# Kernel tuning notes

Measured on AMD Instinct MI355X. Metric: run time of the kernel, lower is better.

## Reference

```python
import jax, jax.numpy as jnp
import numpy as np

N = 50000
E = 800000
G_DIM = 512
H1 = 128
H2 = 128
R = 8  # 2 * n_speakers**2


def setup_inputs() -> dict:
    key = jax.random.key(0)
    ks = jax.random.split(key, 16)
    s = lambda d: 1.0 / np.sqrt(d)
    inp = {
        'node_features': jax.random.normal(ks[0], (N, G_DIM), jnp.float32),
        'edge_index': jax.random.randint(ks[1], (2, E), 0, N, jnp.int64),
        'edge_type': jax.random.randint(ks[2], (E,), 0, R, jnp.int64),
        # RGCNConv params
        'W_rel': jax.random.normal(ks[3], (R, G_DIM, H1), jnp.float32) * s(G_DIM),
        'W_root': jax.random.normal(ks[4], (G_DIM, H1), jnp.float32) * s(G_DIM),
        'b1': jnp.zeros((H1,), jnp.float32),
        # TransformerConv params (heads=1)
        'Wq': jax.random.normal(ks[5], (H1, H2), jnp.float32) * s(H1),
        'bq': jnp.zeros((H2,), jnp.float32),
        'Wk': jax.random.normal(ks[6], (H1, H2), jnp.float32) * s(H1),
        'bk': jnp.zeros((H2,), jnp.float32),
        'Wv': jax.random.normal(ks[7], (H1, H2), jnp.float32) * s(H1),
        'bv': jnp.zeros((H2,), jnp.float32),
        'Wskip': jax.random.normal(ks[8], (H1, H2), jnp.float32) * s(H1),
        'bskip': jnp.zeros((H2,), jnp.float32),
        # BatchNorm1d params
        'gamma': jnp.ones((H2,), jnp.float32),
        'beta': jnp.zeros((H2,), jnp.float32),
    }
    return inp


def reference(node_features, edge_index, edge_type, W_rel, W_root, b1,
              Wq, bq, Wk, bk, Wv, bv, Wskip, bskip, gamma, beta):
    n = node_features.shape[0]
    r = W_rel.shape[0]
    src, dst = edge_index[0], edge_index[1]

    # ---- RGCNConv: per-relation mean aggregation + root + bias ----
    # x @ W_r for all relations, then per-edge gather: [n,r,h1] -> [E,h1]
    xW = jnp.einsum('nf,rfh->nrh', node_features, W_rel)
    msg = xW[src, edge_type]                         # [E, H1]
    comp = dst * r + edge_type                       # composite (node, relation) key
    cnt = jax.ops.segment_sum(jnp.ones((msg.shape[0],), msg.dtype), comp,
                              num_segments=n * r)
    denom = jnp.maximum(cnt[comp], 1.0)[:, None]     # mean within each (node, rel)
    agg1 = jax.ops.segment_sum(msg / denom, dst, num_segments=n)
    h = agg1 + node_features @ W_root + b1           # [n, H1]

    # ---- TransformerConv (heads=1): segment-softmax attention ----
    q = h @ Wq + bq
    k = h @ Wk + bk
    v = h @ Wv + bv
    d = q.shape[-1]
    score = jnp.sum(q[dst] * k[src], axis=-1) / jnp.sqrt(jnp.float32(d))  # [E]
    smax = jax.ops.segment_max(score, dst, num_segments=n)
    smax = jnp.where(jnp.isfinite(smax), smax, 0.0)
    ex = jnp.exp(score - smax[dst])
    ssum = jax.ops.segment_sum(ex, dst, num_segments=n)
    alpha = ex / jnp.maximum(ssum[dst], 1e-16)       # [E]
    agg2 = jax.ops.segment_sum(alpha[:, None] * v[src], dst, num_segments=n)
    h2 = agg2 + h @ Wskip + bskip                    # root (lin_skip) path

    # ---- BatchNorm1d (training mode: batch stats) + LeakyReLU(0.01) ----
    mu = jnp.mean(h2, axis=0)
    var = jnp.mean((h2 - mu) ** 2, axis=0)
    xn = (h2 - mu) / jnp.sqrt(var + 1e-5)
    out = gamma * xn + beta
    return jnp.where(out >= 0, out, 0.01 * out)
```

## Files before the change

kernel.cpp:

```cpp
#include <hip/hip_runtime.h>

typedef float f32x4 __attribute__((ext_vector_type(4)));
typedef _Float16 f16x8 __attribute__((ext_vector_type(8)));

#define NN 50000
#define EE 800000
#define GD 512
#define H1C 128
#define RR 8
#define NC1 1152
#define NC2 512
#define SCAN_BLK 256
#define NCAST (NN * GD / 4)

__device__ __forceinline__ unsigned short f2h(float f){
  _Float16 h = (_Float16)f;
  unsigned short u; __builtin_memcpy(&u, &h, 2); return u;
}
__device__ __forceinline__ float h2f(unsigned short u){
  _Float16 h; __builtin_memcpy(&h, &u, 2); return (float)h;
}
__device__ __forceinline__ void gload16(const void* g, void* l){
  __builtin_amdgcn_global_load_lds(
      (const __attribute__((address_space(1))) unsigned int*)g,
      (__attribute__((address_space(3))) unsigned int*)l, 16, 0, 0);
}

__global__ void k_prep(unsigned* __restrict__ zp, int nzero,
                       const float* __restrict__ x, unsigned short* __restrict__ x16,
                       const float* __restrict__ W_rel, const float* __restrict__ W_root,
                       unsigned short* __restrict__ wcatT,
                       const float* __restrict__ Wq, const float* __restrict__ Wk,
                       const float* __restrict__ Wv, const float* __restrict__ Ws,
                       const float* __restrict__ bq, const float* __restrict__ bk,
                       const float* __restrict__ bv, const float* __restrict__ bs,
                       unsigned short* __restrict__ w2T, float* __restrict__ bias2){
  int i = blockIdx.x * 256 + threadIdx.x;
  if (i < nzero){ zp[i] = 0u; return; }
  i -= nzero;
  if (i < NCAST){
    int b = i * 4;
    float4 v = *(const float4*)(x + b);
    ushort4 o;
    o.x = f2h(v.x); o.y = f2h(v.y); o.z = f2h(v.z); o.w = f2h(v.w);
    *(ushort4*)(x16 + b) = o;
    return;
  }
  i -= NCAST;
  if (i < NC1 * GD){
    int j = i >> 9;
    int f = i & 511;
    float v;
    if (j < 1024) v = W_rel[((size_t)(j >> 7) * GD + f) * H1C + (j & 127)];
    else          v = W_root[(size_t)f * H1C + (j - 1024)];
    wcatT[(size_t)j * GD + f] = f2h(v);
    return;
  }
  i -= NC1 * GD;
  if (i < NC2 * H1C){
    int j = i >> 7;
    int f = i & 127;
    int m = j >> 7;
    int hc = j & 127;
    const float* W = (m == 0) ? Wq : (m == 1) ? Wk : (m == 2) ? Wv : Ws;
    w2T[(size_t)j * H1C + f] = f2h(W[(size_t)f * H1C + hc]);
    if (f == 0){
      const float* B = (m == 0) ? bq : (m == 1) ? bk : (m == 2) ? bv : bs;
      bias2[j] = B[hc];
    }
  }
}

__global__ void k_hist(const int* __restrict__ ei, const int* __restrict__ et,
                       float* __restrict__ cnt, int E){
  int e = blockIdx.x * blockDim.x + threadIdx.x;
  if (e >= E) return;
  atomicAdd(&cnt[(size_t)ei[E + e] * RR + et[e]], 1.0f);
}

__global__ void k_scan_partial(const float* __restrict__ cnt, int* __restrict__ deg,
                               int* __restrict__ bsum, int n){
  __shared__ int s[SCAN_BLK];
  int i = blockIdx.x * SCAN_BLK + threadIdx.x;
  int dv = 0;
  if (i < n){
    const float4* c = (const float4*)(cnt + (size_t)i * 8);
    float4 a = c[0], b = c[1];
    float fs = a.x + a.y + a.z + a.w + b.x + b.y + b.z + b.w;
    dv = (int)(fs + 0.5f);
    deg[i] = dv;
  }
  s[threadIdx.x] = dv;
  __syncthreads();
  for (int off = 128; off >= 1; off >>= 1){
    if (threadIdx.x < off) s[threadIdx.x] += s[threadIdx.x + off];
    __syncthreads();
  }
  if (threadIdx.x == 0) bsum[blockIdx.x] = s[0];
}

__global__ void k_scan_top(int* __restrict__ bsum, int* __restrict__ boff, int nb){
  __shared__ int s[SCAN_BLK];
  int t = threadIdx.x;
  int v = (t < nb) ? bsum[t] : 0;
  s[t] = v;
  __syncthreads();
  #pragma unroll
  for (int off = 1; off < SCAN_BLK; off <<= 1){
    int tv = (t >= off) ? s[t - off] : 0;
    __syncthreads();
    s[t] += tv;
    __syncthreads();
  }
  if (t < nb) boff[t] = s[t] - v;
}

__global__ void k_scan_final(const int* __restrict__ deg, const int* __restrict__ boff,
                             int* __restrict__ base, int n){
  __shared__ int s[SCAN_BLK];
  int i = blockIdx.x * SCAN_BLK + threadIdx.x;
  int t = threadIdx.x;
  int v = (i < n) ? deg[i] : 0;
  s[t] = v;
  __syncthreads();
  #pragma unroll
  for (int off = 1; off < SCAN_BLK; off <<= 1){
    int tv = (t >= off) ? s[t - off] : 0;
    __syncthreads();
    s[t] += tv;
    __syncthreads();
  }
  if (i < n) base[i] = s[t] - v + boff[blockIdx.x];
}

__global__ void k_scatter_perm(const int* __restrict__ ei, const int* __restrict__ et,
                               const int* __restrict__ base, int* __restrict__ cursor,
                               unsigned* __restrict__ sortedSR, int E){
  int e = blockIdx.x * blockDim.x + threadIdx.x;
  if (e >= E) return;
  int dst = ei[E + e];
  int pos = base[dst] + atomicAdd(&cursor[dst], 1);
  sortedSR[pos] = (unsigned)(ei[e] & 0xFFFF) | ((unsigned)et[e] << 16);
}

#define TILE 128
#define BK 64

__global__ __launch_bounds__(256) void k_gemm(
    const unsigned short* __restrict__ A,
    const unsigned short* __restrict__ Bt,
    unsigned short* __restrict__ C,
    const float* __restrict__ bias,
    int M, int Nout, int K, int rowsPerXcd, int colBlocks)
{
  int bid = blockIdx.x;
  int xcd = bid & 7;
  int lin = bid >> 3;
  int rowb = xcd * rowsPerXcd + lin / colBlocks;
  int colb = lin % colBlocks;
  int row0 = rowb * TILE;
  if (row0 >= M) return;
  int col0 = colb * TILE;

  __shared__ unsigned short As[TILE][BK];
  __shared__ unsigned short Bs[TILE][BK];
  int tid = threadIdx.x;
  int wave = tid >> 6, lane = tid & 63;
  int wm = (wave >> 1) * 64, wn = (wave & 1) * 64;
  int l16 = lane & 15, quad = lane >> 4;

  int srow = lane >> 3;
  int gcb  = ((lane & 7) ^ srow) * 8;
  int xorr = l16 & 7;

  f32x4 acc[4][4] = {};

  for (int k0 = 0; k0 < K; k0 += BK){
    __syncthreads();
    #pragma unroll
    for (int i = 0; i < 4; i++){
      int rbase = (wave * 4 + i) * 8;
      int gr = row0 + rbase + srow; if (gr >= M) gr = M - 1;
      gload16(A + (size_t)gr * K + k0 + gcb, &As[rbase][0]);
    }
    #pragma unroll
    for (int i = 0; i < 4; i++){
      int rbase = (wave * 4 + i) * 8;
      int gc = col0 + rbase + srow;
      gload16(Bt + (size_t)gc * K + k0 + gcb, &Bs[rbase][0]);
    }
    __syncthreads();
    #pragma unroll
    for (int ks = 0; ks < BK; ks += 32){
      int scol = ((quad + (ks >> 3)) ^ xorr) * 8;
      f16x8 af[4], bfr[4];
      #pragma unroll
      for (int i = 0; i < 4; i++) af[i] = *(const f16x8*)&As[wm + i*16 + l16][scol];
      #pragma unroll
      for (int j = 0; j < 4; j++) bfr[j] = *(const f16x8*)&Bs[wn + j*16 + l16][scol];
      #pragma unroll
      for (int i = 0; i < 4; i++)
        #pragma unroll
        for (int j = 0; j < 4; j++)
          acc[i][j] = __builtin_amdgcn_mfma_f32_16x16x32_f16(af[i], bfr[j], acc[i][j], 0, 0, 0);
    }
  }

  #pragma unroll
  for (int i = 0; i < 4; i++){
    int rbase = row0 + wm + i*16 + quad*4;
    #pragma unroll
    for (int j = 0; j < 4; j++){
      int col = col0 + wn + j*16 + l16;
      float b = bias ? bias[col] : 0.0f;
      #pragma unroll
      for (int rr = 0; rr < 4; rr++){
        int row = rbase + rr;
        if (row < M) C[(size_t)row * Nout + col] = f2h(acc[i][j][rr] + b);
      }
    }
  }
}

__global__ __launch_bounds__(256) void k_rgcn_seg(
    const int* __restrict__ base, const int* __restrict__ deg,
    const unsigned* __restrict__ srt,
    const unsigned short* __restrict__ xW, const float* __restrict__ cnt,
    const float* __restrict__ b1, unsigned short* __restrict__ h16)
{
  int v = blockIdx.x * 4 + (threadIdx.x >> 6);
  if (v >= NN) return;
  int lane = threadIdx.x & 63;
  int g = lane >> 4, l16 = lane & 15;
  int start = base[v], d = deg[v];
  const float* cv = cnt + (size_t)v * RR;

  float o[8] = {};
  for (int cb = 0; cb < d; cb += 16){
    int srcs[4]; int rels[4]; float invs[4];
    #pragma unroll
    for (int t = 0; t < 4; t++){
      int idx = cb + 4 * t + g;
      bool valid = idx < d;
      unsigned sri = valid ? srt[start + idx] : 0u;
      srcs[t] = (int)(sri & 0xFFFFu);
      rels[t] = (int)(sri >> 16);
      invs[t] = valid ? 1.0f / fmaxf(cv[rels[t]], 1.0f) : 0.0f;
    }
    uint4 u[4];
    #pragma unroll
    for (int t = 0; t < 4; t++)
      u[t] = *(const uint4*)(xW + (size_t)srcs[t] * NC1 + rels[t] * H1C + l16 * 8);
    #pragma unroll
    for (int t = 0; t < 4; t++){
      const unsigned short* p = (const unsigned short*)&u[t];
      #pragma unroll
      for (int j = 0; j < 8; j++) o[j] += h2f(p[j]) * invs[t];
    }
  }
  #pragma unroll
  for (int j = 0; j < 8; j++){
    o[j] += __shfl_xor(o[j], 16, 64);
    o[j] += __shfl_xor(o[j], 32, 64);
  }
  if (g == 0){
    uint4 r = *(const uint4*)(xW + (size_t)v * NC1 + 1024 + l16 * 8);
    const unsigned short* p = (const unsigned short*)&r;
    unsigned short res[8];
    #pragma unroll
    for (int j = 0; j < 8; j++) res[j] = f2h(o[j] + h2f(p[j]) + b1[l16 * 8 + j]);
    *(uint4*)(h16 + (size_t)v * H1C + l16 * 8) = *(uint4*)res;
  }
}

__global__ __launch_bounds__(256) void k_attn3(
    const int* __restrict__ base, const int* __restrict__ deg,
    const unsigned* __restrict__ srt,
    const unsigned short* __restrict__ qkvs, float* __restrict__ h2)
{
  int v = blockIdx.x * 4 + (threadIdx.x >> 6);
  if (v >= NN) return;
  int lane = threadIdx.x & 63;
  int g = lane >> 4, l16 = lane & 15;
  int start = base[v], d = deg[v];
  const float sc = 0.08838834764831845f;

  float qf[8];
  {
    uint4 qa = *(const uint4*)(qkvs + (size_t)v * NC2 + l16 * 8);
    const unsigned short* p = (const unsigned short*)&qa;
    #pragma unroll
    for (int i = 0; i < 8; i++) qf[i] = h2f(p[i]);
  }

  float o[8] = {};
  float m = -INFINITY, l = 0.0f;

  for (int cb = 0; cb < d; cb += 16){
    int srcs[4]; bool val[4];
    #pragma unroll
    for (int t = 0; t < 4; t++){
      int idx = cb + 4 * t + g;
      val[t] = idx < d;
      srcs[t] = val[t] ? (int)(srt[start + idx] & 0xFFFFu) : 0;
    }
    uint4 ka[4], va[4];
    #pragma unroll
    for (int t = 0; t < 4; t++)
      ka[t] = *(const uint4*)(qkvs + (size_t)srcs[t] * NC2 + 128 + l16 * 8);
    #pragma unroll
    for (int t = 0; t < 4; t++)
      va[t] = *(const uint4*)(qkvs + (size_t)srcs[t] * NC2 + 256 + l16 * 8);

    float s[4];
    #pragma unroll
    for (int t = 0; t < 4; t++){
      const unsigned short* p = (const unsigned short*)&ka[t];
      float ss = 0.0f;
      #pragma unroll
      for (int i = 0; i < 8; i++) ss += qf[i] * h2f(p[i]);
      #pragma unroll
      for (int off = 8; off >= 1; off >>= 1) ss += __shfl_xor(ss, off, 16);
      s[t] = val[t] ? ss * sc : -INFINITY;
    }

    float m4 = fmaxf(fmaxf(s[0], s[1]), fmaxf(s[2], s[3]));
    m4 = fmaxf(m4, __shfl_xor(m4, 16, 64));
    m4 = fmaxf(m4, __shfl_xor(m4, 32, 64));
    float newm = fmaxf(m, m4);
    float scale = __expf(m - newm);
    float e[4], esum = 0.0f;
    #pragma unroll
    for (int t = 0; t < 4; t++){
      e[t] = val[t] ? __expf(s[t] - newm) : 0.0f;
      esum += e[t];
    }
    esum += __shfl_xor(esum, 16, 64);
    esum += __shfl_xor(esum, 32, 64);
    l = l * scale + esum;

    #pragma unroll
    for (int j = 0; j < 8; j++) o[j] *= scale;
    #pragma unroll
    for (int t = 0; t < 4; t++){
      const unsigned short* p = (const unsigned short*)&va[t];
      #pragma unroll
      for (int j = 0; j < 8; j++) o[j] += e[t] * h2f(p[j]);
    }
    m = newm;
  }

  #pragma unroll
  for (int j = 0; j < 8; j++){
    o[j] += __shfl_xor(o[j], 16, 64);
    o[j] += __shfl_xor(o[j], 32, 64);
  }
  if (g == 0){
    float r = (d > 0) ? 1.0f / fmaxf(l, 1e-16f) : 0.0f;
    uint4 sk = *(const uint4*)(qkvs + (size_t)v * NC2 + 384 + l16 * 8);
    const unsigned short* p = (const unsigned short*)&sk;
    float* hd = h2 + (size_t)v * H1C + l16 * 8;
    float4 r0 = make_float4(h2f(p[0]) + o[0]*r, h2f(p[1]) + o[1]*r,
                            h2f(p[2]) + o[2]*r, h2f(p[3]) + o[3]*r);
    float4 r1 = make_float4(h2f(p[4]) + o[4]*r, h2f(p[5]) + o[5]*r,
                            h2f(p[6]) + o[6]*r, h2f(p[7]) + o[7]*r);
    *(float4*)hd = r0;
    *(float4*)(hd + 4) = r1;
  }
}

__global__ __launch_bounds__(256) void k_bn_reduce(const float* __restrict__ h2,
                                                   float* __restrict__ bn, int Nrows){
  __shared__ float ls[256], lq[256];
  int c = threadIdx.x & 127;
  int half = threadIdx.x >> 7;
  float s = 0.0f, q = 0.0f;
  for (int r = blockIdx.x * 2 + half; r < Nrows; r += gridDim.x * 2){
    float v = h2[(size_t)r * H1C + c];
    s += v; q += v * v;
  }
  ls[threadIdx.x] = s; lq[threadIdx.x] = q;
  __syncthreads();
  if (half == 0){
    atomicAdd(&bn[c],        ls[c] + ls[c + 128]);
    atomicAdd(&bn[128 + c],  lq[c] + lq[c + 128]);
  }
}

__global__ void k_out(const float* __restrict__ h2, const float* __restrict__ bn,
                      const float* __restrict__ gamma, const float* __restrict__ beta,
                      float* __restrict__ out, int n, float invN){
  int idx = blockIdx.x * blockDim.x + threadIdx.x;
  if (idx >= n) return;
  int c = idx & 127;
  float mu = bn[c] * invN;
  float var = bn[128 + c] * invN - mu * mu;
  float rs = rsqrtf(var + 1e-5f);
  float v = (h2[idx] - mu) * rs;
  float o = gamma[c] * v + beta[c];
  out[idx] = (o >= 0.0f) ? o : 0.01f * o;
}

extern "C" void kernel_launch(void* const* d_in, const int* in_sizes, int n_in,
                              void* d_out, int out_size, void* d_ws, size_t ws_size,
                              hipStream_t stream) {
  const float* x      = (const float*)d_in[0];
  const int*   ei     = (const int*)d_in[1];
  const int*   et     = (const int*)d_in[2];
  const float* W_rel  = (const float*)d_in[3];
  const float* W_root = (const float*)d_in[4];
  const float* b1     = (const float*)d_in[5];
  const float* Wq     = (const float*)d_in[6];
  const float* bq     = (const float*)d_in[7];
  const float* Wk     = (const float*)d_in[8];
  const float* bk     = (const float*)d_in[9];
  const float* Wv     = (const float*)d_in[10];
  const float* bv     = (const float*)d_in[11];
  const float* Wskip  = (const float*)d_in[12];
  const float* bskip  = (const float*)d_in[13];
  const float* gamma  = (const float*)d_in[14];
  const float* beta   = (const float*)d_in[15];
  float* out = (float*)d_out;

  const int N = NN, E = EE;
  char* ws = (char*)d_ws;
  size_t off = 0;
  auto alloc = [&](size_t bytes){ size_t r = off; off = (off + bytes + 255) & ~(size_t)255; return r; };

  size_t o_x16   = alloc((size_t)N * GD * 2);
  size_t o_w1    = alloc((size_t)NC1 * GD * 2);
  size_t o_xw    = alloc((size_t)N * NC1 * 2);
  size_t o_cnt   = alloc((size_t)N * RR * 4);
  size_t o_cur   = alloc((size_t)N * 4);
  size_t o_bn    = alloc((size_t)512 * 4);
  size_t o_zend  = off;
  size_t o_deg   = alloc((size_t)N * 4);
  size_t o_base  = alloc((size_t)N * 4);
  size_t o_bsum  = alloc((size_t)SCAN_BLK * 4);
  size_t o_boff  = alloc((size_t)SCAN_BLK * 4);
  size_t o_srt   = alloc((size_t)E * 4);
  size_t o_h16   = alloc((size_t)N * H1C * 2);
  size_t o_w2    = alloc((size_t)NC2 * H1C * 2);
  size_t o_b2    = alloc((size_t)NC2 * 4);

  unsigned short* x16   = (unsigned short*)(ws + o_x16);
  unsigned short* qkvs  = (unsigned short*)(ws + o_x16);
  unsigned short* wcatT = (unsigned short*)(ws + o_w1);
  unsigned short* xW    = (unsigned short*)(ws + o_xw);
  float*          h2    = (float*)(ws + o_xw);
  float*          cnt   = (float*)(ws + o_cnt);
  int*            cursor= (int*)(ws + o_cur);
  float*          bn    = (float*)(ws + o_bn);
  int*            deg   = (int*)(ws + o_deg);
  int*            basea = (int*)(ws + o_base);
  int*            bsum  = (int*)(ws + o_bsum);
  int*            boff  = (int*)(ws + o_boff);
  unsigned*       srt   = (unsigned*)(ws + o_srt);
  unsigned short* h16   = (unsigned short*)(ws + o_h16);
  unsigned short* w2T   = (unsigned short*)(ws + o_w2);
  float*          bias2 = (float*)(ws + o_b2);

  const int TPB = 256;
  const int NBLK = (N + SCAN_BLK - 1) / SCAN_BLK;
  const int ROWB = (N + TILE - 1) / TILE;
  const int RPX  = (ROWB + 7) / 8;

  int nzero = (int)((o_zend - o_cnt) / 4);
  long prepN = (long)nzero + NCAST + NC1 * GD + NC2 * H1C;
  k_prep<<<(prepN + TPB - 1) / TPB, TPB, 0, stream>>>(
      (unsigned*)(ws + o_cnt), nzero, x, x16, W_rel, W_root, wcatT,
      Wq, Wk, Wv, Wskip, bq, bk, bv, bskip, w2T, bias2);

  k_hist<<<(E + TPB - 1) / TPB, TPB, 0, stream>>>(ei, et, cnt, E);
  k_scan_partial<<<NBLK, SCAN_BLK, 0, stream>>>(cnt, deg, bsum, N);
  k_scan_top<<<1, SCAN_BLK, 0, stream>>>(bsum, boff, NBLK);
  k_scan_final<<<NBLK, SCAN_BLK, 0, stream>>>(deg, boff, basea, N);
  k_scatter_perm<<<(E + TPB - 1) / TPB, TPB, 0, stream>>>(ei, et, basea, cursor, srt, E);

  k_gemm<<<8 * RPX * (NC1 / TILE), TPB, 0, stream>>>(x16, wcatT, xW, nullptr, N, NC1, GD, RPX, NC1 / TILE);

  k_rgcn_seg<<<(N + 3) / 4, TPB, 0, stream>>>(basea, deg, srt, xW, cnt, b1, h16);

  k_gemm<<<8 * RPX * (NC2 / TILE), TPB, 0, stream>>>(h16, w2T, qkvs, bias2, N, NC2, H1C, RPX, NC2 / TILE);

  k_attn3<<<(N + 3) / 4, TPB, 0, stream>>>(basea, deg, srt, qkvs, h2);

  k_bn_reduce<<<256, TPB, 0, stream>>>(h2, bn, N);
  k_out<<<((size_t)N * H1C + TPB - 1) / TPB, TPB, 0, stream>>>(h2, bn, gamma, beta, out, N * H1C, 1.0f / N);
}
```

Measured before the change: 569.9 us.

## Fuse histogram into GEMM launch, replace scan with atomic allocation, use fdot2

```diff
diff --git a/kernel.cpp b/kernel.cpp
--- a/kernel.cpp
+++ b/kernel.cpp
@@ -2,6 +2,7 @@
 
 typedef float f32x4 __attribute__((ext_vector_type(4)));
 typedef _Float16 f16x8 __attribute__((ext_vector_type(8)));
+typedef _Float16 f16x2 __attribute__((ext_vector_type(2)));
 
 #define NN 50000
 #define EE 800000
@@ -10,7 +11,6 @@
 #define RR 8
 #define NC1 1152
 #define NC2 512
-#define SCAN_BLK 256
 #define NCAST (NN * GD / 4)
 
 __device__ __forceinline__ unsigned short f2h(float f){
@@ -24,6 +24,13 @@
   __builtin_amdgcn_global_load_lds(
       (const __attribute__((address_space(1))) unsigned int*)g,
       (__attribute__((address_space(3))) unsigned int*)l, 16, 0, 0);
+}
+__device__ __forceinline__ float dot2(f16x2 a, f16x2 b, float c){
+#if __has_builtin(__builtin_amdgcn_fdot2)
+  return __builtin_amdgcn_fdot2(a, b, c, false);
+#else
+  return c + (float)a[0] * (float)b[0] + (float)a[1] * (float)b[1];
+#endif
 }
 
 __global__ void k_prep(unsigned* __restrict__ zp, int nzero,
@@ -71,75 +78,26 @@
   }
 }
 
-__global__ void k_hist(const int* __restrict__ ei, const int* __restrict__ et,
-                       float* __restrict__ cnt, int E){
-  int e = blockIdx.x * blockDim.x + threadIdx.x;
-  if (e >= E) return;
-  atomicAdd(&cnt[(size_t)ei[E + e] * RR + et[e]], 1.0f);
-}
-
-__global__ void k_scan_partial(const float* __restrict__ cnt, int* __restrict__ deg,
-                               int* __restrict__ bsum, int n){
-  __shared__ int s[SCAN_BLK];
-  int i = blockIdx.x * SCAN_BLK + threadIdx.x;
-  int dv = 0;
-  if (i < n){
-    const float4* c = (const float4*)(cnt + (size_t)i * 8);
-    float4 a = c[0], b = c[1];
-    float fs = a.x + a.y + a.z + a.w + b.x + b.y + b.z + b.w;
-    dv = (int)(fs + 0.5f);
-    deg[i] = dv;
-  }
-  s[threadIdx.x] = dv;
-  __syncthreads();
-  for (int off = 128; off >= 1; off >>= 1){
-    if (threadIdx.x < off) s[threadIdx.x] += s[threadIdx.x + off];
-    __syncthreads();
-  }
-  if (threadIdx.x == 0) bsum[blockIdx.x] = s[0];
-}
-
-__global__ void k_scan_top(int* __restrict__ bsum, int* __restrict__ boff, int nb){
-  __shared__ int s[SCAN_BLK];
-  int t = threadIdx.x;
-  int v = (t < nb) ? bsum[t] : 0;
-  s[t] = v;
-  __syncthreads();
-  #pragma unroll
-  for (int off = 1; off < SCAN_BLK; off <<= 1){
-    int tv = (t >= off) ? s[t - off] : 0;
-    __syncthreads();
-    s[t] += tv;
-    __syncthreads();
-  }
-  if (t < nb) boff[t] = s[t] - v;
-}
-
-__global__ void k_scan_final(const int* __restrict__ deg, const int* __restrict__ boff,
-                             int* __restrict__ base, int n){
-  __shared__ int s[SCAN_BLK];
-  int i = blockIdx.x * SCAN_BLK + threadIdx.x;
-  int t = threadIdx.x;
-  int v = (i < n) ? deg[i] : 0;
-  s[t] = v;
-  __syncthreads();
-  #pragma unroll
-  for (int off = 1; off < SCAN_BLK; off <<= 1){
-    int tv = (t >= off) ? s[t - off] : 0;
-    __syncthreads();
-    s[t] += tv;
-    __syncthreads();
-  }
-  if (i < n) base[i] = s[t] - v + boff[blockIdx.x];
+__global__ void k_alloc(const float* __restrict__ cnt, int* __restrict__ deg,
+                        int* __restrict__ basea, int* __restrict__ cur,
+                        unsigned* __restrict__ total, int n){
+  int v = blockIdx.x * 256 + threadIdx.x;
+  if (v >= n) return;
+  const float4* c = (const float4*)(cnt + (size_t)v * 8);
+  float4 a = c[0], b = c[1];
+  int d = (int)(a.x + a.y + a.z + a.w + b.x + b.y + b.z + b.w + 0.5f);
+  deg[v] = d;
+  int base = (int)atomicAdd(total, (unsigned)d);
+  basea[v] = base;
+  cur[v] = base;
 }
 
 __global__ void k_scatter_perm(const int* __restrict__ ei, const int* __restrict__ et,
-                               const int* __restrict__ base, int* __restrict__ cursor,
-                               unsigned* __restrict__ sortedSR, int E){
+                               int* __restrict__ cur, unsigned* __restrict__ sortedSR, int E){
   int e = blockIdx.x * blockDim.x + threadIdx.x;
   if (e >= E) return;
   int dst = ei[E + e];
-  int pos = base[dst] + atomicAdd(&cursor[dst], 1);
+  int pos = atomicAdd(&cur[dst], 1);
   sortedSR[pos] = (unsigned)(ei[e] & 0xFFFF) | ((unsigned)et[e] << 16);
 }
 
@@ -151,9 +109,16 @@
     const unsigned short* __restrict__ Bt,
     unsigned short* __restrict__ C,
     const float* __restrict__ bias,
-    int M, int Nout, int K, int rowsPerXcd, int colBlocks)
+    int M, int Nout, int K, int rowsPerXcd, int colBlocks,
+    int gemmBlocks, const int* __restrict__ ei, const int* __restrict__ et,
+    float* __restrict__ cnt, int E)
 {
   int bid = blockIdx.x;
+  if (bid >= gemmBlocks){
+    int e = (bid - gemmBlocks) * 256 + threadIdx.x;
+    if (e < E) atomicAdd(&cnt[(size_t)ei[E + e] * RR + et[e]], 1.0f);
+    return;
+  }
   int xcd = bid & 7;
   int lin = bid >> 3;
   int rowb = xcd * rowsPerXcd + lin / colBlocks;
@@ -285,13 +250,8 @@
   int start = base[v], d = deg[v];
   const float sc = 0.08838834764831845f;
 
-  float qf[8];
-  {
-    uint4 qa = *(const uint4*)(qkvs + (size_t)v * NC2 + l16 * 8);
-    const unsigned short* p = (const unsigned short*)&qa;
-    #pragma unroll
-    for (int i = 0; i < 8; i++) qf[i] = h2f(p[i]);
-  }
+  uint4 qa = *(const uint4*)(qkvs + (size_t)v * NC2 + l16 * 8);
+  const f16x2* qh = (const f16x2*)&qa;
 
   float o[8] = {};
   float m = -INFINITY, l = 0.0f;
@@ -315,10 +275,10 @@
     float s[4];
     #pragma unroll
     for (int t = 0; t < 4; t++){
-      const unsigned short* p = (const unsigned short*)&ka[t];
+      const f16x2* kh = (const f16x2*)&ka[t];
       float ss = 0.0f;
       #pragma unroll
-      for (int i = 0; i < 8; i++) ss += qf[i] * h2f(p[i]);
+      for (int i = 0; i < 4; i++) ss = dot2(qh[i], kh[i], ss);
       #pragma unroll
       for (int off = 8; off >= 1; off >>= 1) ss += __shfl_xor(ss, off, 16);
       s[t] = val[t] ? ss * sc : -INFINITY;
@@ -431,13 +391,12 @@
   size_t o_w1    = alloc((size_t)NC1 * GD * 2);
   size_t o_xw    = alloc((size_t)N * NC1 * 2);
   size_t o_cnt   = alloc((size_t)N * RR * 4);
-  size_t o_cur   = alloc((size_t)N * 4);
   size_t o_bn    = alloc((size_t)512 * 4);
+  size_t o_tot   = alloc((size_t)64 * 4);
   size_t o_zend  = off;
   size_t o_deg   = alloc((size_t)N * 4);
   size_t o_base  = alloc((size_t)N * 4);
-  size_t o_bsum  = alloc((size_t)SCAN_BLK * 4);
-  size_t o_boff  = alloc((size_t)SCAN_BLK * 4);
+  size_t o_cur   = alloc((size_t)N * 4);
   size_t o_srt   = alloc((size_t)E * 4);
   size_t o_h16   = alloc((size_t)N * H1C * 2);
   size_t o_w2    = alloc((size_t)NC2 * H1C * 2);
@@ -449,21 +408,20 @@
   unsigned short* xW    = (unsigned short*)(ws + o_xw);
   float*          h2    = (float*)(ws + o_xw);
   float*          cnt   = (float*)(ws + o_cnt);
-  int*            cursor= (int*)(ws + o_cur);
   float*          bn    = (float*)(ws + o_bn);
+  unsigned*       total = (unsigned*)(ws + o_tot);
   int*            deg   = (int*)(ws + o_deg);
   int*            basea = (int*)(ws + o_base);
-  int*            bsum  = (int*)(ws + o_bsum);
-  int*            boff  = (int*)(ws + o_boff);
+  int*            cur   = (int*)(ws + o_cur);
   unsigned*       srt   = (unsigned*)(ws + o_srt);
   unsigned short* h16   = (unsigned short*)(ws + o_h16);
   unsigned short* w2T   = (unsigned short*)(ws + o_w2);
   float*          bias2 = (float*)(ws + o_b2);
 
   const int TPB = 256;
-  const int NBLK = (N + SCAN_BLK - 1) / SCAN_BLK;
   const int ROWB = (N + TILE - 1) / TILE;
   const int RPX  = (ROWB + 7) / 8;
+  const int HISTB = (E + TPB - 1) / TPB;
 
   int nzero = (int)((o_zend - o_cnt) / 4);
   long prepN = (long)nzero + NCAST + NC1 * GD + NC2 * H1C;
@@ -471,17 +429,22 @@
       (unsigned*)(ws + o_cnt), nzero, x, x16, W_rel, W_root, wcatT,
       Wq, Wk, Wv, Wskip, bq, bk, bv, bskip, w2T, bias2);
 
-  k_hist<<<(E + TPB - 1) / TPB, TPB, 0, stream>>>(ei, et, cnt, E);
-  k_scan_partial<<<NBLK, SCAN_BLK, 0, stream>>>(cnt, deg, bsum, N);
-  k_scan_top<<<1, SCAN_BLK, 0, stream>>>(bsum, boff, NBLK);
-  k_scan_final<<<NBLK, SCAN_BLK, 0, stream>>>(deg, boff, basea, N);
-  k_scatter_perm<<<(E + TPB - 1) / TPB, TPB, 0, stream>>>(ei, et, basea, cursor, srt, E);
-
-  k_gemm<<<8 * RPX * (NC1 / TILE), TPB, 0, stream>>>(x16, wcatT, xW, nullptr, N, NC1, GD, RPX, NC1 / TILE);
+  {
+    int gemmB = 8 * RPX * (NC1 / TILE);
+    k_gemm<<<gemmB + HISTB, TPB, 0, stream>>>(x16, wcatT, xW, nullptr,
+        N, NC1, GD, RPX, NC1 / TILE, gemmB, ei, et, cnt, E);
+  }
+
+  k_alloc<<<(N + TPB - 1) / TPB, TPB, 0, stream>>>(cnt, deg, basea, cur, total, N);
+  k_scatter_perm<<<HISTB, TPB, 0, stream>>>(ei, et, cur, srt, E);
 
   k_rgcn_seg<<<(N + 3) / 4, TPB, 0, stream>>>(basea, deg, srt, xW, cnt, b1, h16);
 
-  k_gemm<<<8 * RPX * (NC2 / TILE), TPB, 0, stream>>>(h16, w2T, qkvs, bias2, N, NC2, H1C, RPX, NC2 / TILE);
+  {
+    int gemmB = 8 * RPX * (NC2 / TILE);
+    k_gemm<<<gemmB, TPB, 0, stream>>>(h16, w2T, qkvs, bias2,
+        N, NC2, H1C, RPX, NC2 / TILE, gemmB, nullptr, nullptr, cnt, 0);
+  }
 
   k_attn3<<<(N + 3) / 4, TPB, 0, stream>>>(basea, deg, srt, qkvs, h2);
 
```

Result: no change. 563.4 us (-1.2%).
